# Kernel tuning notes

Measured on AMD Instinct MI355X. Metric: run time of the kernel, lower is better.

The kernel has to match this reference:

```python
import jax, jax.numpy as jnp
import numpy as np

N, D, E, TOP_K = 16384, 1024, 8, 2

def setup_inputs() -> dict:
    key = jax.random.key(0)
    ks = jax.random.split(key, 8)
    sc = 1.0 / np.sqrt(D)
    return {
        "x": jax.random.normal(ks[0], (N, D), dtype=jnp.float32),
        "context_vector": jax.random.uniform(ks[1], (E,), dtype=jnp.float32),
        "router_w": jax.random.uniform(ks[2], (E, D), minval=-sc, maxval=sc),
        "router_b": jax.random.uniform(ks[3], (E,), minval=-sc, maxval=sc),
        "expert_w": jax.random.uniform(ks[4], (E, D, D), minval=-sc, maxval=sc),
        "expert_b": jax.random.uniform(ks[5], (E, D), minval=-sc, maxval=sc),
        "context_weight": jax.random.uniform(ks[6], (1,), dtype=jnp.float32),
    }

def reference(x, context_vector, router_w, router_b, expert_w, expert_b, context_weight):
    # Router: gate logits with conceptual context bias. [N, E]
    gate_logits = x @ router_w.T + router_b + context_weight * context_vector
    weights = jax.nn.softmax(gate_logits, axis=-1)

    # Top-k selection and renormalization. [N, k]
    top_k_weights, top_k_indices = jax.lax.top_k(weights, TOP_K)
    top_k_weights = top_k_weights / jnp.sum(top_k_weights, axis=-1, keepdims=True)

    # All-expert outputs (dense grouped GEMM): y[n,e,:] = x[n] @ W[e].T + b[e]
    all_out = jnp.einsum('nd,efd->nef', x, expert_w) + expert_b  # [N, E, D]

    # Gather the top-k expert outputs per token and combine. [N, k, D]
    gathered = jnp.take_along_axis(all_out, top_k_indices[:, :, None], axis=1)
    expert_outputs = jnp.sum(top_k_weights[:, :, None] * gathered, axis=1)  # [N, D]

    # Load-balancing loss: avg router prob . fraction of tokens routed per expert
    avg_router_prob = weights.mean(axis=0)  # [E]
    assignment_mask = jax.nn.one_hot(top_k_indices, E).sum(axis=1)  # [N, E]
    fraction_routed = assignment_mask.mean(axis=0)  # [E]
    load_loss = jnp.sum(avg_router_prob * fraction_routed)

    return expert_outputs, load_loss
```

## Files before the change

kernel.cpp:

```cpp
#include <hip/hip_runtime.h>
#include <stdint.h>

#define N_TOK 16384
#define DDIM  1024
#define NEXP  8
#define CNT_STRIDE 64

#define BM 256
#define BN 256
#define BK 64
#define NKT 16
#define MAX_TILES 136
#define EP_PITCH 72

typedef __bf16 bf16x8 __attribute__((ext_vector_type(8)));
typedef float  f32x4  __attribute__((ext_vector_type(4)));

__device__ __forceinline__ unsigned short f2bf(float f) {
  union { float f; uint32_t u; } a; a.f = f;
  uint32_t u = a.u;
  u += 0x7fffu + ((u >> 16) & 1u);
  return (unsigned short)(u >> 16);
}

__device__ __forceinline__ float bf2f(unsigned short u) {
  union { uint32_t u; float f; } a; a.u = ((uint32_t)u) << 16;
  return a.f;
}

__device__ __forceinline__ float2 bfpair(uint32_t u) {
  union { uint32_t u; float f; } lo, hi;
  lo.u = u << 16; hi.u = u & 0xffff0000u;
  return make_float2(lo.f, hi.f);
}

__device__ __forceinline__ void load_lds16(const void* g, void* l) {
  __builtin_amdgcn_global_load_lds(
      (const __attribute__((address_space(1))) void*)g,
      (__attribute__((address_space(3))) void*)l,
      16, 0, 0);
}

#define SCHED_FENCE() __builtin_amdgcn_sched_barrier(0)
#define BAR_PLAIN() do { SCHED_FENCE(); asm volatile("s_barrier" ::: "memory"); SCHED_FENCE(); } while (0)
#define BAR_VM0()   do { SCHED_FENCE(); asm volatile("s_waitcnt vmcnt(0)\n\ts_barrier" ::: "memory"); SCHED_FENCE(); } while (0)

__global__ __launch_bounds__(512) void router_kernel(
    const float* __restrict__ x, const float* __restrict__ rw,
    const float* __restrict__ rb, const float* __restrict__ cv,
    const float* __restrict__ cwp,
    const float4* __restrict__ ew4, ushort4* __restrict__ wb4,
    unsigned short* __restrict__ xg,
    int* __restrict__ perm_idx, float* __restrict__ perm_w,
    int* __restrict__ inv_idx,
    int* __restrict__ cnt, float* __restrict__ sum_w)
{
  __shared__ int   sCnt[NEXP];
  __shared__ int   sBase[NEXP];
  __shared__ float sSW[NEXP];
  __shared__ int   sE0[32], sE1[32], sR0[32], sR1[32];
  __shared__ float sW0[32], sW1[32];

  const int tid = threadIdx.x;
  if (tid < NEXP) { sCnt[tid] = 0; sSW[tid] = 0.0f; }
  __syncthreads();

  const int wave = tid >> 6;
  const int lane = tid & 63;

  float lsw[NEXP];
#pragma unroll
  for (int e = 0; e < NEXP; ++e) lsw[e] = 0.0f;

  const float cw = cwp[0];

  for (int t = 0; t < 4; ++t) {
    const int i = wave * 4 + t;
    const int n = blockIdx.x * 32 + i;

    float p[NEXP];
#pragma unroll
    for (int e = 0; e < NEXP; ++e) p[e] = 0.0f;

    const float2* x2 = (const float2*)(x + (size_t)n * DDIM);
    uint32_t* xgp = (uint32_t*)(xg + (size_t)n * DDIM);

    float2 xv[8];
#pragma unroll
    for (int it = 0; it < 8; ++it) xv[it] = x2[lane + 64 * it];
#pragma unroll
    for (int it = 0; it < 8; ++it) {
      int dp = lane + 64 * it;
      xgp[dp] = (uint32_t)f2bf(xv[it].x) | ((uint32_t)f2bf(xv[it].y) << 16);
#pragma unroll
      for (int e = 0; e < NEXP; ++e) {
        float2 wv = ((const float2*)(rw + e * DDIM))[dp];
        p[e] = fmaf(xv[it].x, wv.x, fmaf(xv[it].y, wv.y, p[e]));
      }
    }
#pragma unroll
    for (int e = 0; e < NEXP; ++e) {
#pragma unroll
      for (int off = 32; off > 0; off >>= 1)
        p[e] += __shfl_xor(p[e], off, 64);
    }

    if (lane == 0) {
      float w[NEXP];
      float m = -1e30f;
#pragma unroll
      for (int e = 0; e < NEXP; ++e) {
        w[e] = p[e] + rb[e] + cw * cv[e];
        m = fmaxf(m, w[e]);
      }
      float s = 0.0f;
#pragma unroll
      for (int e = 0; e < NEXP; ++e) { w[e] = expf(w[e] - m); s += w[e]; }
      float inv = 1.0f / s;
#pragma unroll
      for (int e = 0; e < NEXP; ++e) { w[e] *= inv; lsw[e] += w[e]; }
      int e0 = 0;
#pragma unroll
      for (int e = 1; e < NEXP; ++e) if (w[e] > w[e0]) e0 = e;
      int e1 = (e0 == 0) ? 1 : 0;
#pragma unroll
      for (int e = 0; e < NEXP; ++e) if (e != e0 && w[e] > w[e1]) e1 = e;
      float rsum = 1.0f / (w[e0] + w[e1]);
      int r0 = atomicAdd(&sCnt[e0], 1);
      int r1 = atomicAdd(&sCnt[e1], 1);
      sE0[i] = e0; sE1[i] = e1; sR0[i] = r0; sR1[i] = r1;
      sW0[i] = w[e0] * rsum; sW1[i] = w[e1] * rsum;
    }
  }

  if (lane == 0) {
#pragma unroll
    for (int e = 0; e < NEXP; ++e) atomicAdd(&sSW[e], lsw[e]);
  }
  __syncthreads();

  if (tid < NEXP) {
    sBase[tid] = atomicAdd(&cnt[tid * CNT_STRIDE], sCnt[tid]);
    atomicAdd(&sum_w[tid * CNT_STRIDE], sSW[tid]);
  }
  __syncthreads();

  if (tid < 64) {
    int i = tid >> 1, k = tid & 1;
    int e = k ? sE1[i] : sE0[i];
    int r = k ? sR1[i] : sR0[i];
    float wv = k ? sW1[i] : sW0[i];
    int pos = sBase[e] + r;
    int n = blockIdx.x * 32 + i;
    perm_idx[e * N_TOK + pos] = n;
    perm_w [e * N_TOK + pos] = wv;
    inv_idx[2 * n + k] = (e << 14) | pos;
  }

  size_t base = (size_t)blockIdx.x * 512 + tid;
#pragma unroll
  for (int i2 = 0; i2 < 8; ++i2) {
    size_t idx = base + (size_t)i2 * 262144;
    float4 v = ew4[idx];
    wb4[idx] = make_ushort4(f2bf(v.x), f2bf(v.y), f2bf(v.z), f2bf(v.w));
  }
}

template<int MODE>
__global__ __launch_bounds__(512, 2) void moe_gemm_kernel(
    const unsigned short* __restrict__ xg, const unsigned short* __restrict__ wb,
    const float* __restrict__ eb,
    const int* __restrict__ perm_idx, const float* __restrict__ perm_w,
    const int* __restrict__ cnt,
    unsigned short* __restrict__ ybuf, float* __restrict__ out)
{
  const int id = blockIdx.x;
  const int tn = id / MAX_TILES;
  const int tileIdx = id - tn * MAX_TILES;

  int e = -1, tm = 0, count = 0, ebase = 0, pref = 0;
#pragma unroll
  for (int j = 0; j < NEXP; ++j) {
    int c = cnt[j * CNT_STRIDE];
    int t = (c + BM - 1) >> 8;
    if (e < 0 && tileIdx < pref + t) { e = j; tm = tileIdx - pref; count = c; }
    if (e < 0) ebase += c;
    pref += t;
  }
  if (e < 0) return;

  __shared__ union {
    struct { __bf16 As[2][BM * BK]; __bf16 Bs[2][BN * BK]; } g;
    __bf16 ep[8 * 64 * EP_PITCH];
  } sm;
  __shared__ int   tokS[BM];
  __shared__ float wtS[BM];

  const int tid = threadIdx.x;
  const int wave = tid >> 6;
  const int lane = tid & 63;

  if (tid < BM) {
    int row = tm * BM + tid;
    int rc = row < count ? row : count - 1;
    tokS[tid] = perm_idx[e * N_TOK + rc];
    wtS[tid] = (row < count) ? perm_w[e * N_TOK + row] : 0.0f;
  }
  __syncthreads();

  const unsigned short* wbase = wb + (size_t)e * DDIM * DDIM;
  const int rl = wave * 16 + (lane >> 3);
  const int cg = (((lane & 7) ^ (lane >> 3)) & 7) * 8;

  const unsigned short* gA[2][2];
  const unsigned short* gB[2][2];
#pragma unroll
  for (int h = 0; h < 2; ++h)
#pragma unroll
    for (int j = 0; j < 2; ++j) {
      gA[h][j] = xg + (size_t)tokS[h * 128 + rl + j * 8] * DDIM + cg;
      gB[h][j] = wbase + (size_t)(tn * BN + h * 128 + rl + j * 8) * DDIM + cg;
    }

#define STG_A(h, bsel) do { \
    load_lds16(gA[h][0], &sm.g.As[bsel][((h) * 128 + wave * 16) * BK]);     gA[h][0] += BK; \
    load_lds16(gA[h][1], &sm.g.As[bsel][((h) * 128 + wave * 16 + 8) * BK]); gA[h][1] += BK; \
  } while (0)
#define STG_B(h, bsel) do { \
    load_lds16(gB[h][0], &sm.g.Bs[bsel][((h) * 128 + wave * 16) * BK]);     gB[h][0] += BK; \
    load_lds16(gB[h][1], &sm.g.Bs[bsel][((h) * 128 + wave * 16 + 8) * BK]); gB[h][1] += BK; \
  } while (0)

  STG_A(0, 0); STG_A(1, 0); STG_B(0, 0); STG_B(1, 0);
  BAR_VM0();

  const int wr = wave >> 2;
  const int wc = wave & 3;
  const int quad = lane >> 4;
  const int l15 = lane & 15;
  const int sl0 = (quad ^ (l15 & 7)) * 8;
  const int rowA = (wr * 128 + l15) * BK + sl0;
  const int rowB = (wc * 64 + l15) * BK + sl0;

  f32x4 acc[8][4] = {};

#pragma unroll
  for (int t = 0; t < NKT; ++t) {
    const int b = t & 1, nb = b ^ 1;
    const __bf16* Ab = sm.g.As[b];
    const __bf16* Bb = sm.g.Bs[b];

    if (t + 1 < NKT) { STG_A(0, nb); STG_A(1, nb); STG_B(0, nb); STG_B(1, nb); }

    bf16x8 Bf[4][2];
#pragma unroll
    for (int ni = 0; ni < 4; ++ni)
#pragma unroll
      for (int ks = 0; ks < 2; ++ks)
        Bf[ni][ks] = *(const bf16x8*)&Bb[(rowB + ni * 1024) ^ (ks * 32)];

#pragma unroll
    for (int mi = 0; mi < 8; ++mi) {
      bf16x8 a0 = *(const bf16x8*)&Ab[(rowA + mi * 1024)];
      bf16x8 a1 = *(const bf16x8*)&Ab[(rowA + mi * 1024) ^ 32];
#pragma unroll
      for (int ni = 0; ni < 4; ++ni) {
        acc[mi][ni] = __builtin_amdgcn_mfma_f32_16x16x32_bf16(Bf[ni][0], a0, acc[mi][ni], 0, 0, 0);
        acc[mi][ni] = __builtin_amdgcn_mfma_f32_16x16x32_bf16(Bf[ni][1], a1, acc[mi][ni], 0, 0, 0);
      }
    }

    if (t + 1 < NKT) BAR_VM0();
    else             BAR_PLAIN();
  }

#undef STG_A
#undef STG_B

  const int valid = count - tm * BM;
  const int gb = ebase + tm * BM;

  if (MODE == 1) {
    __bf16* slab = &sm.ep[wave * (64 * EP_PITCH)];
#pragma unroll
    for (int p = 0; p < 2; ++p) {
#pragma unroll
      for (int mi4 = 0; mi4 < 4; ++mi4) {
        const int mi = p * 4 + mi4;
        float wt = wtS[wr * 128 + mi * 16 + l15];
#pragma unroll
        for (int ni = 0; ni < 4; ++ni) {
          int gcol = tn * BN + wc * 64 + ni * 16 + quad * 4;
          const float4 bv = *(const float4*)&eb[e * DDIM + gcol];
          ushort4 pk;
          pk.x = f2bf((acc[mi][ni][0] + bv.x) * wt);
          pk.y = f2bf((acc[mi][ni][1] + bv.y) * wt);
          pk.z = f2bf((acc[mi][ni][2] + bv.z) * wt);
          pk.w = f2bf((acc[mi][ni][3] + bv.w) * wt);
          *(ushort4*)&slab[(mi4 * 16 + l15) * EP_PITCH + ni * 16 + quad * 4] = pk;
        }
      }
#pragma unroll
      for (int s = 0; s < 8; ++s) {
        int lrow = s * 8 + (lane >> 3);
        uint4 v = *(const uint4*)&slab[lrow * EP_PITCH + (lane & 7) * 8];
        int brow = wr * 128 + p * 64 + lrow;
        if (brow < valid)
          *(uint4*)&ybuf[(size_t)(gb + brow) * DDIM + tn * BN + wc * 64 + (lane & 7) * 8] = v;
      }
    }
  } else {
#pragma unroll
    for (int mi = 0; mi < 8; ++mi) {
      int brow = wr * 128 + mi * 16 + l15;
      float wt = wtS[brow];
      int tok = tokS[brow];
      if (brow < valid) {
#pragma unroll
        for (int ni = 0; ni < 4; ++ni) {
          int gcol = tn * BN + wc * 64 + ni * 16 + quad * 4;
          const float4 bv = *(const float4*)&eb[e * DDIM + gcol];
          atomicAdd(out + (size_t)tok * DDIM + gcol + 0, (acc[mi][ni][0] + bv.x) * wt);
          atomicAdd(out + (size_t)tok * DDIM + gcol + 1, (acc[mi][ni][1] + bv.y) * wt);
          atomicAdd(out + (size_t)tok * DDIM + gcol + 2, (acc[mi][ni][2] + bv.z) * wt);
          atomicAdd(out + (size_t)tok * DDIM + gcol + 3, (acc[mi][ni][3] + bv.w) * wt);
        }
      }
    }
  }
}

__global__ __launch_bounds__(256) void combine_kernel(
    const unsigned short* __restrict__ ybuf, const int* __restrict__ inv_idx,
    const int* __restrict__ cnt, float* __restrict__ out)
{
  const int wave = threadIdx.x >> 6;
  const int lane = threadIdx.x & 63;
  const int n = blockIdx.x * 4 + wave;

  int base[NEXP];
  int acc = 0;
#pragma unroll
  for (int j = 0; j < NEXP; ++j) { base[j] = acc; acc += cnt[j * CNT_STRIDE]; }

  int i0 = inv_idx[2 * n];
  int i1 = inv_idx[2 * n + 1];
  int g0 = base[i0 >> 14] + (i0 & 16383);
  int g1 = base[i1 >> 14] + (i1 & 16383);

  const uint4* r0 = (const uint4*)(ybuf + (size_t)g0 * DDIM);
  const uint4* r1 = (const uint4*)(ybuf + (size_t)g1 * DDIM);
  float4* o = (float4*)(out + (size_t)n * DDIM);

#pragma unroll
  for (int it = 0; it < 2; ++it) {
    int c = lane + 64 * it;
    uint4 a = r0[c];
    uint4 b = r1[c];
    float2 a0 = bfpair(a.x), a1 = bfpair(a.y), a2 = bfpair(a.z), a3 = bfpair(a.w);
    float2 b0 = bfpair(b.x), b1 = bfpair(b.y), b2 = bfpair(b.z), b3 = bfpair(b.w);
    float4 v0, v1;
    v0.x = a0.x + b0.x; v0.y = a0.y + b0.y; v0.z = a1.x + b1.x; v0.w = a1.y + b1.y;
    v1.x = a2.x + b2.x; v1.y = a2.y + b2.y; v1.z = a3.x + b3.x; v1.w = a3.y + b3.y;
    o[2 * c] = v0;
    o[2 * c + 1] = v1;
  }
}

__global__ void loss_kernel(const float* __restrict__ sum_w,
                            const int* __restrict__ cnt,
                            float* __restrict__ out) {
  if (threadIdx.x == 0 && blockIdx.x == 0) {
    float l = 0.0f;
#pragma unroll
    for (int e = 0; e < NEXP; ++e)
      l += sum_w[e * CNT_STRIDE] * (float)cnt[e * CNT_STRIDE];
    out[(size_t)N_TOK * DDIM] = l * (1.0f / ((float)N_TOK * (float)N_TOK));
  }
}

extern "C" void kernel_launch(void* const* d_in, const int* in_sizes, int n_in,
                              void* d_out, int out_size, void* d_ws, size_t ws_size,
                              hipStream_t stream) {
  const float* x  = (const float*)d_in[0];
  const float* cv = (const float*)d_in[1];
  const float* rw = (const float*)d_in[2];
  const float* rb = (const float*)d_in[3];
  const float* ew = (const float*)d_in[4];
  const float* eb = (const float*)d_in[5];
  const float* cw = (const float*)d_in[6];
  float* out = (float*)d_out;

  char* ws = (char*)d_ws;
  unsigned short* xg = (unsigned short*)ws;
  unsigned short* wb = (unsigned short*)(ws + 33554432);
  int*   perm_idx = (int*)  (ws + 50331648);
  float* perm_w   = (float*)(ws + 50855936);
  int*   inv_idx  = (int*)  (ws + 51380224);
  int*   cnt      = (int*)  (ws + 51511296);
  float* sum_w    = (float*)(ws + 51513344);
  unsigned short* ybuf = (unsigned short*)(ws + 51515392);
  const size_t NEED = 51515392ull + 67108864ull;

  const bool big = ws_size >= NEED;

  hipMemsetAsync(cnt, 0, 4096, stream);
  if (!big)
    hipMemsetAsync(d_out, 0, (size_t)N_TOK * DDIM * sizeof(float), stream);

  router_kernel<<<N_TOK / 32, 512, 0, stream>>>(x, rw, rb, cv, cw,
                                                (const float4*)ew, (ushort4*)wb,
                                                xg, perm_idx, perm_w, inv_idx, cnt, sum_w);

  if (big) {
    moe_gemm_kernel<1><<<MAX_TILES * 4, 512, 0, stream>>>(
        xg, wb, eb, perm_idx, perm_w, cnt, ybuf, out);
    combine_kernel<<<N_TOK / 4, 256, 0, stream>>>(ybuf, inv_idx, cnt, out);
  } else {
    moe_gemm_kernel<0><<<MAX_TILES * 4, 512, 0, stream>>>(
        xg, wb, eb, perm_idx, perm_w, cnt, ybuf, out);
  }

  loss_kernel<<<1, 64, 0, stream>>>(sum_w, cnt, out);
}
```

Baseline: 284.8 us.

## Split expert weight cast into own kernel; batch router tokens per wave

Moves the fp32-to-bf16 expert weight conversion out of the router kernel into a separate cast kernel. The router now processes four tokens per wave together with float4 loads, so each router weight vector is loaded once per iteration and reused across the four tokens instead of being reloaded per token. This reduces redundant router-weight traffic and shortens the router kernel, at the cost of one extra kernel launch and more registers held per thread for four tokens' partial sums.

Result: slower. 291.5 us (+2.4%).

```diff
diff --git a/kernel.cpp b/kernel.cpp
--- a/kernel.cpp
+++ b/kernel.cpp
@@ -45,11 +45,22 @@
 #define BAR_PLAIN() do { SCHED_FENCE(); asm volatile("s_barrier" ::: "memory"); SCHED_FENCE(); } while (0)
 #define BAR_VM0()   do { SCHED_FENCE(); asm volatile("s_waitcnt vmcnt(0)\n\ts_barrier" ::: "memory"); SCHED_FENCE(); } while (0)
 
+__global__ __launch_bounds__(256) void castw_kernel(
+    const float4* __restrict__ ew4, ushort4* __restrict__ wb4)
+{
+  size_t idx = (size_t)blockIdx.x * 256 + threadIdx.x;
+#pragma unroll
+  for (int i = 0; i < 4; ++i) {
+    float4 v = ew4[idx];
+    wb4[idx] = make_ushort4(f2bf(v.x), f2bf(v.y), f2bf(v.z), f2bf(v.w));
+    idx += 524288;
+  }
+}
+
 __global__ __launch_bounds__(512) void router_kernel(
     const float* __restrict__ x, const float* __restrict__ rw,
     const float* __restrict__ rb, const float* __restrict__ cv,
     const float* __restrict__ cwp,
-    const float4* __restrict__ ew4, ushort4* __restrict__ wb4,
     unsigned short* __restrict__ xg,
     int* __restrict__ perm_idx, float* __restrict__ perm_w,
     int* __restrict__ inv_idx,
@@ -67,50 +78,69 @@
 
   const int wave = tid >> 6;
   const int lane = tid & 63;
+  const int n0 = blockIdx.x * 32 + wave * 4;
+
+  const float cw = cwp[0];
+  const float4* rw4 = (const float4*)rw;
+
+  const float4* x4[4];
+  uint2* xgp[4];
+#pragma unroll
+  for (int t = 0; t < 4; ++t) {
+    x4[t]  = (const float4*)(x + (size_t)(n0 + t) * DDIM);
+    xgp[t] = (uint2*)(xg + (size_t)(n0 + t) * DDIM);
+  }
+
+  float p[4][NEXP];
+#pragma unroll
+  for (int t = 0; t < 4; ++t)
+#pragma unroll
+    for (int e = 0; e < NEXP; ++e) p[t][e] = 0.0f;
+
+#pragma unroll
+  for (int it = 0; it < 4; ++it) {
+    const int dp = lane + 64 * it;
+    float4 wv[NEXP];
+#pragma unroll
+    for (int e = 0; e < NEXP; ++e) wv[e] = rw4[e * 256 + dp];
+#pragma unroll
+    for (int t = 0; t < 4; ++t) {
+      float4 xv = x4[t][dp];
+      uint2 pk;
+      pk.x = (uint32_t)f2bf(xv.x) | ((uint32_t)f2bf(xv.y) << 16);
+      pk.y = (uint32_t)f2bf(xv.z) | ((uint32_t)f2bf(xv.w) << 16);
+      xgp[t][dp] = pk;
+#pragma unroll
+      for (int e = 0; e < NEXP; ++e)
+        p[t][e] = fmaf(xv.x, wv[e].x,
+                  fmaf(xv.y, wv[e].y,
+                  fmaf(xv.z, wv[e].z,
+                  fmaf(xv.w, wv[e].w, p[t][e]))));
+    }
+  }
+
+#pragma unroll
+  for (int t = 0; t < 4; ++t)
+#pragma unroll
+    for (int e = 0; e < NEXP; ++e) {
+#pragma unroll
+      for (int off = 32; off > 0; off >>= 1)
+        p[t][e] += __shfl_xor(p[t][e], off, 64);
+    }
 
   float lsw[NEXP];
 #pragma unroll
   for (int e = 0; e < NEXP; ++e) lsw[e] = 0.0f;
 
-  const float cw = cwp[0];
-
+#pragma unroll
   for (int t = 0; t < 4; ++t) {
     const int i = wave * 4 + t;
-    const int n = blockIdx.x * 32 + i;
-
-    float p[NEXP];
-#pragma unroll
-    for (int e = 0; e < NEXP; ++e) p[e] = 0.0f;
-
-    const float2* x2 = (const float2*)(x + (size_t)n * DDIM);
-    uint32_t* xgp = (uint32_t*)(xg + (size_t)n * DDIM);
-
-    float2 xv[8];
-#pragma unroll
-    for (int it = 0; it < 8; ++it) xv[it] = x2[lane + 64 * it];
-#pragma unroll
-    for (int it = 0; it < 8; ++it) {
-      int dp = lane + 64 * it;
-      xgp[dp] = (uint32_t)f2bf(xv[it].x) | ((uint32_t)f2bf(xv[it].y) << 16);
-#pragma unroll
-      for (int e = 0; e < NEXP; ++e) {
-        float2 wv = ((const float2*)(rw + e * DDIM))[dp];
-        p[e] = fmaf(xv[it].x, wv.x, fmaf(xv[it].y, wv.y, p[e]));
-      }
-    }
-#pragma unroll
-    for (int e = 0; e < NEXP; ++e) {
-#pragma unroll
-      for (int off = 32; off > 0; off >>= 1)
-        p[e] += __shfl_xor(p[e], off, 64);
-    }
-
     if (lane == 0) {
       float w[NEXP];
       float m = -1e30f;
 #pragma unroll
       for (int e = 0; e < NEXP; ++e) {
-        w[e] = p[e] + rb[e] + cw * cv[e];
+        w[e] = p[t][e] + rb[e] + cw * cv[e];
         m = fmaxf(m, w[e]);
       }
       float s = 0.0f;
@@ -155,14 +185,6 @@
     perm_idx[e * N_TOK + pos] = n;
     perm_w [e * N_TOK + pos] = wv;
     inv_idx[2 * n + k] = (e << 14) | pos;
-  }
-
-  size_t base = (size_t)blockIdx.x * 512 + tid;
-#pragma unroll
-  for (int i2 = 0; i2 < 8; ++i2) {
-    size_t idx = base + (size_t)i2 * 262144;
-    float4 v = ew4[idx];
-    wb4[idx] = make_ushort4(f2bf(v.x), f2bf(v.y), f2bf(v.z), f2bf(v.w));
   }
 }
 
@@ -408,8 +430,9 @@
   if (!big)
     hipMemsetAsync(d_out, 0, (size_t)N_TOK * DDIM * sizeof(float), stream);
 
+  castw_kernel<<<2048, 256, 0, stream>>>((const float4*)ew, (ushort4*)wb);
+
   router_kernel<<<N_TOK / 32, 512, 0, stream>>>(x, rw, rb, cv, cw,
-                                                (const float4*)ew, (ushort4*)wb,
                                                 xg, perm_idx, perm_w, inv_idx, cnt, sum_w);
 
   if (big) {
```
